# Optimization experiments

Hardware: AMD Instinct MI355X
Metric: run time of the kernel (lower is better)

## Reference

```python
import jax, jax.numpy as jnp
import numpy as np

SHARP = 50.0  # softness of the analytic brush edge


def _rasterize(param, dec, ps):
    # param: [N,12], dec: [N] float 0/1 -> fg,[N,3,ps,ps] (color*alpha*dec), alpha [N,3,ps,ps]
    p = jax.nn.sigmoid(param[:, :8])
    x0, y0 = p[:, 0], p[:, 1]
    wd = jnp.maximum(p[:, 2], 1e-2)
    ht = jnp.maximum(p[:, 3], 1e-2)
    theta = p[:, 4] * jnp.pi
    color = p[:, 5:8]
    lin = (jnp.arange(ps, dtype=param.dtype) + 0.5) / ps
    gy, gx = jnp.meshgrid(lin, lin, indexing='ij')            # [ps,ps]
    dx = gx[None] - x0[:, None, None]
    dy = gy[None] - y0[:, None, None]
    ct = jnp.cos(theta)[:, None, None]
    st = jnp.sin(theta)[:, None, None]
    u = dx * ct + dy * st
    v = -dx * st + dy * ct
    alpha = (jax.nn.sigmoid(SHARP * (wd[:, None, None] / 2 - jnp.abs(u)))
             * jax.nn.sigmoid(SHARP * (ht[:, None, None] / 2 - jnp.abs(v))))
    alpha = alpha * dec[:, None, None]                         # masked scatter == multiply
    alpha3 = jnp.broadcast_to(alpha[:, None], (alpha.shape[0], 3, ps, ps))
    fg = color[:, :, None, None] * alpha3                      # foreground*alpha pre-fused
    return fg, alpha3


def reference(param, decision, cur_canvas):
    b, h, w, s, _ = param.shape
    H, W = cur_canvas.shape[-2], cur_canvas.shape[-1]
    ps = 2 * H // h  # patch_size (== 2*W//w)
    dec = decision.astype(cur_canvas.dtype).reshape(-1)
    fg, al = _rasterize(param.reshape(-1, 12), dec, ps)
    fg = fg.reshape(b, h, w, s, 3, ps, ps)
    al = al.reshape(b, h, w, s, 3, ps, ps)
    q = ps // 4
    canvas = jnp.pad(cur_canvas, ((0, 0), (0, 0), (q, q), (q, q)))
    ey, ex = np.arange(0, h, 2), np.arange(0, w, 2)
    oy, ox = np.arange(1, h, 2), np.arange(1, w, 2)

    def blend(cv, rows, cols, off_y, off_x):
        ny, nx = len(rows), len(cols)
        region = cv[:, :, off_y:off_y + ny * ps, off_x:off_x + nx * ps]
        tiles = region.reshape(b, 3, ny, ps, nx, ps).transpose(0, 2, 4, 1, 3, 5)  # [b,ny,nx,3,ps,ps]
        sf = fg[:, rows][:, :, cols]   # [b,ny,nx,s,3,ps,ps]
        sa = al[:, rows][:, :, cols]
        for i in range(s):
            tiles = sf[:, :, :, i] + tiles * (1.0 - sa[:, :, :, i])
        region = tiles.transpose(0, 3, 1, 4, 2, 5).reshape(b, 3, ny * ps, nx * ps)
        return cv.at[:, :, off_y:off_y + ny * ps, off_x:off_x + nx * ps].set(region)

    canvas = blend(canvas, ey, ex, 0, 0)
    canvas = blend(canvas, oy, ox, ps // 2, ps // 2)
    canvas = blend(canvas, oy, ex, ps // 2, 0)
    canvas = blend(canvas, ey, ox, 0, ps // 2)
    return canvas[:, :, q:-q, q:-q]


def setup_inputs() -> dict:
    key = jax.random.key(0)
    k1, k2, k3 = jax.random.split(key, 3)
    b, h, w, s = 1, 64, 64, 5
    H = W = 1024
    param = jax.random.normal(k1, (b, h, w, s, 12), dtype=jnp.float32)
    decision = jax.random.randint(k2, (b, h, w, s), 0, 2, dtype=jnp.int32)
    cur_canvas = jax.random.uniform(k3, (b, 3, H, W), dtype=jnp.float32)
    return {'param': param, 'decision': decision, 'cur_canvas': cur_canvas}
```

## Files before the change

### kernel.cpp

```cpp
#include <hip/hip_runtime.h>

#define PI_F 3.14159265358979323846f
constexpr float SL = 50.0f * 1.44269504089f;

__device__ __forceinline__ float fexp2(float x) {
#if __has_builtin(__builtin_amdgcn_exp2f)
  return __builtin_amdgcn_exp2f(x);
#else
  return __expf(x * 0.69314718056f);
#endif
}
__device__ __forceinline__ float frcp(float x) {
#if __has_builtin(__builtin_amdgcn_rcpf)
  return __builtin_amdgcn_rcpf(x);
#else
  return 1.0f / x;
#endif
}
__device__ __forceinline__ float fsig(float x) {
  return frcp(1.0f + fexp2(-x * 1.44269504089f));
}

__global__ __launch_bounds__(64) void render_kernel(
    const float* __restrict__ param, const int* __restrict__ dec,
    const float* __restrict__ canvas, float* __restrict__ out) {
  __shared__ float4 lds4[20 * 3];

  const int A = blockIdx.y, B = blockIdx.x;
  const int re = (A & 1) ? A - 1 : A;
  const int ro = (A & 1) ? A : A - 1;
  const int ce = (B & 1) ? B - 1 : B;
  const int co = (B & 1) ? B : B - 1;

  const int j = threadIdx.x;

  bool live = false;
  float4 w0q, w1q, w2q;
  if (j < 20) {
    const int k = j / 5;
    const int i = j - k * 5;
    const int rr = (k == 0 || k == 3) ? re : ro;
    const int cc = (k & 1) ? co : ce;
    if ((unsigned)rr < 64u && (unsigned)cc < 64u) {
      const int tid = rr * 64 + cc;
      const int sid = tid * 5 + i;
      if (dec[sid] != 0) {
        const float4* p4 = (const float4*)(param + (size_t)sid * 12);
        float4 a = p4[0];
        float4 b = p4[1];
        float x0 = fsig(a.x), y0 = fsig(a.y);
        float wd = fmaxf(fsig(a.z), 0.01f);
        float ht = fmaxf(fsig(a.w), 0.01f);
        float th = fsig(b.x) * PI_F;
        float ct = __cosf(th), st = __sinf(th);
        w0q = make_float4((float)(cc * 16) + 32.0f * x0,
                          (float)(rr * 16) + 32.0f * y0,
                          ct * (SL / 32.0f), st * (SL / 32.0f));
        w1q = make_float4(SL * wd * 0.5f, SL * ht * 0.5f,
                          fsig(b.y), fsig(b.z));
        w2q = make_float4(fsig(b.w), 0.0f, 0.0f, 0.0f);
        live = true;
      }
    }
  }
  const unsigned long long mask = __ballot(live);
  const int total = __popcll(mask);
  if (live) {
    const int off = __popcll(mask & ((1ull << j) - 1));
    lds4[off * 3 + 0] = w0q;
    lds4[off * 3 + 1] = w1q;
    lds4[off * 3 + 2] = w2q;
  }
  __syncthreads();

  const int cg = j & 3;
  const int row = j >> 2;
  const int Xb = B * 16 - 8 + cg * 4;
  const int Yr = A * 16 - 8 + row;
  const bool valid = ((unsigned)Xb < 1024u) & ((unsigned)Yr < 1024u);
  if (!valid) return;

  const size_t pix = (size_t)Yr * 1024 + Xb;
  float4 v0 = *(const float4*)(canvas + pix);
  float4 v1 = *(const float4*)(canvas + pix + 1024 * 1024);
  float4 v2 = *(const float4*)(canvas + pix + 2 * 1024 * 1024);

  const float fx0 = (float)(B * 16 + cg * 4) + 0.5f;
  const float fy  = (float)(A * 16 + row) + 0.5f;

  for (int s = 0; s < total; ++s) {
    const float4 qa = lds4[s * 3 + 0];
    const float4 qb = lds4[s * 3 + 1];
    const float4 qc = lds4[s * 3 + 2];
    const float dx0 = fx0 - qa.x;
    const float dy  = fy - qa.y;
    float u = dx0 * qa.z + dy * qa.w;
    float w = dy * qa.z - dx0 * qa.w;
    float* pv0 = &v0.x;
    float* pv1 = &v1.x;
    float* pv2 = &v2.x;
#pragma unroll
    for (int m = 0; m < 4; ++m) {
      const float e1 = fexp2(fabsf(u) - qb.x);
      const float e2 = fexp2(fabsf(w) - qb.y);
      const float al = frcp((1.0f + e1) * (1.0f + e2));
      pv0[m] = fmaf(al, qb.z - pv0[m], pv0[m]);
      pv1[m] = fmaf(al, qb.w - pv1[m], pv1[m]);
      pv2[m] = fmaf(al, qc.x - pv2[m], pv2[m]);
      u += qa.z;
      w -= qa.w;
    }
  }

  *(float4*)(out + pix) = v0;
  *(float4*)(out + pix + 1024 * 1024) = v1;
  *(float4*)(out + pix + 2 * 1024 * 1024) = v2;
}

extern "C" void kernel_launch(void* const* d_in, const int* in_sizes, int n_in,
                              void* d_out, int out_size, void* d_ws, size_t ws_size,
                              hipStream_t stream) {
  const float* param  = (const float*)d_in[0];
  const int*   dec    = (const int*)d_in[1];
  const float* canvas = (const float*)d_in[2];
  float* outp = (float*)d_out;
  (void)d_ws; (void)ws_size;

  dim3 grid(65, 65, 1);
  render_kernel<<<grid, 64, 0, stream>>>(param, dec, canvas, outp);
}
```

Baseline: 79.58 us.

## Cull negligible strokes, remap blocks across XCDs, hoist canvas loads, unroll by two

Each stroke's alpha is now bounded over the 16x16 block, and strokes whose sigmoid product falls below about 2^-20 everywhere are dropped before blending. Block IDs are remapped so each XCD gets a contiguous range of tiles, which should improve L2 locality. Canvas loads are issued before the stroke setup so their latency overlaps it. The stroke loop is unrolled by two so the exp and rcp work of two strokes can interleave. The __syncthreads is replaced by a bare lgkmcnt wait, which is only safe because the block is a single 64-wide wavefront; culling also adds a small approximation error.

```diff
diff --git a/kernel.cpp b/kernel.cpp
--- a/kernel.cpp
+++ b/kernel.cpp
@@ -24,42 +24,74 @@
 __global__ __launch_bounds__(64) void render_kernel(
     const float* __restrict__ param, const int* __restrict__ dec,
     const float* __restrict__ canvas, float* __restrict__ out) {
-  __shared__ float4 lds4[20 * 3];
+  __shared__ float4 ldsA[20];
+  __shared__ float4 ldsB[20];
+  __shared__ float  ldsC[20];
 
-  const int A = blockIdx.y, B = blockIdx.x;
+  const int bid = blockIdx.y * 65 + blockIdx.x;
+  const int xcd = bid & 7;
+  const int idx = bid >> 3;
+  const int rid = (xcd == 0) ? idx : (529 + (xcd - 1) * 528 + idx);
+  const int A = rid / 65;
+  const int B = rid - A * 65;
+
+  const int j = threadIdx.x;
+
+  const int cg = j & 3;
+  const int row = j >> 2;
+  const int Xb = B * 16 - 8 + cg * 4;
+  const int Yr = A * 16 - 8 + row;
+  const bool valid = ((unsigned)Xb < 1024u) & ((unsigned)Yr < 1024u);
+  const size_t pix = (size_t)Yr * 1024 + Xb;
+  float4 v0 = {}, v1 = {}, v2 = {};
+  if (valid) {
+    v0 = *(const float4*)(canvas + pix);
+    v1 = *(const float4*)(canvas + pix + 1024 * 1024);
+    v2 = *(const float4*)(canvas + pix + 2 * 1024 * 1024);
+  }
+
   const int re = (A & 1) ? A - 1 : A;
   const int ro = (A & 1) ? A : A - 1;
   const int ce = (B & 1) ? B - 1 : B;
   const int co = (B & 1) ? B : B - 1;
 
-  const int j = threadIdx.x;
-
   bool live = false;
-  float4 w0q, w1q, w2q;
+  float4 w0q, w1q;
+  float w2s = 0.0f;
   if (j < 20) {
     const int k = j / 5;
     const int i = j - k * 5;
     const int rr = (k == 0 || k == 3) ? re : ro;
     const int cc = (k & 1) ? co : ce;
     if ((unsigned)rr < 64u && (unsigned)cc < 64u) {
-      const int tid = rr * 64 + cc;
-      const int sid = tid * 5 + i;
-      if (dec[sid] != 0) {
-        const float4* p4 = (const float4*)(param + (size_t)sid * 12);
-        float4 a = p4[0];
-        float4 b = p4[1];
-        float x0 = fsig(a.x), y0 = fsig(a.y);
-        float wd = fmaxf(fsig(a.z), 0.01f);
-        float ht = fmaxf(fsig(a.w), 0.01f);
-        float th = fsig(b.x) * PI_F;
-        float ct = __cosf(th), st = __sinf(th);
-        w0q = make_float4((float)(cc * 16) + 32.0f * x0,
-                          (float)(rr * 16) + 32.0f * y0,
-                          ct * (SL / 32.0f), st * (SL / 32.0f));
-        w1q = make_float4(SL * wd * 0.5f, SL * ht * 0.5f,
-                          fsig(b.y), fsig(b.z));
-        w2q = make_float4(fsig(b.w), 0.0f, 0.0f, 0.0f);
-        live = true;
+      const int sid = (rr * 64 + cc) * 5 + i;
+      const int d = dec[sid];
+      const float4* p4 = (const float4*)(param + (size_t)sid * 12);
+      const float4 a = p4[0];
+      const float4 b = p4[1];
+      if (d != 0) {
+        const float x0 = fsig(a.x), y0 = fsig(a.y);
+        const float wd = fmaxf(fsig(a.z), 0.01f);
+        const float ht = fmaxf(fsig(a.w), 0.01f);
+        const float th = fsig(b.x) * PI_F;
+        const float ct = __cosf(th), st = __sinf(th);
+        const float ctp = ct * (SL / 32.0f), stp = st * (SL / 32.0f);
+        const float X0 = (float)(cc * 16) + 32.0f * x0;
+        const float Y0 = (float)(rr * 16) + 32.0f * y0;
+        const float thU = SL * wd * 0.5f, thV = SL * ht * 0.5f;
+        const float dxc = ((float)(B * 16) + 8.0f) - X0;
+        const float dyc = ((float)(A * 16) + 8.0f) - Y0;
+        const float uc = dxc * ctp + dyc * stp;
+        const float vc = dyc * ctp - dxc * stp;
+        const float dd = (fabsf(ctp) + fabsf(stp)) * 7.5f;
+        const float tu = fminf(thU - fabsf(uc) + dd, 0.0f);
+        const float tv = fminf(thV - fabsf(vc) + dd, 0.0f);
+        if (tu + tv >= -20.0f) {
+          w0q = make_float4(X0, Y0, ctp, stp);
+          w1q = make_float4(thU, thV, fsig(b.y), fsig(b.z));
+          w2s = fsig(b.w);
+          live = true;
+        }
       }
     }
   }
@@ -67,38 +99,66 @@
   const int total = __popcll(mask);
   if (live) {
     const int off = __popcll(mask & ((1ull << j) - 1));
-    lds4[off * 3 + 0] = w0q;
-    lds4[off * 3 + 1] = w1q;
-    lds4[off * 3 + 2] = w2q;
+    ldsA[off] = w0q;
+    ldsB[off] = w1q;
+    ldsC[off] = w2s;
   }
-  __syncthreads();
-
-  const int cg = j & 3;
-  const int row = j >> 2;
-  const int Xb = B * 16 - 8 + cg * 4;
-  const int Yr = A * 16 - 8 + row;
-  const bool valid = ((unsigned)Xb < 1024u) & ((unsigned)Yr < 1024u);
+  asm volatile("s_waitcnt lgkmcnt(0)" ::: "memory");
   if (!valid) return;
-
-  const size_t pix = (size_t)Yr * 1024 + Xb;
-  float4 v0 = *(const float4*)(canvas + pix);
-  float4 v1 = *(const float4*)(canvas + pix + 1024 * 1024);
-  float4 v2 = *(const float4*)(canvas + pix + 2 * 1024 * 1024);
 
   const float fx0 = (float)(B * 16 + cg * 4) + 0.5f;
   const float fy  = (float)(A * 16 + row) + 0.5f;
 
-  for (int s = 0; s < total; ++s) {
-    const float4 qa = lds4[s * 3 + 0];
-    const float4 qb = lds4[s * 3 + 1];
-    const float4 qc = lds4[s * 3 + 2];
-    const float dx0 = fx0 - qa.x;
-    const float dy  = fy - qa.y;
+  float* pv0 = &v0.x;
+  float* pv1 = &v1.x;
+  float* pv2 = &v2.x;
+
+  int s = 0;
+  for (; s + 2 <= total; s += 2) {
+    const float4 qa0 = ldsA[s],     qb0 = ldsB[s];
+    const float4 qa1 = ldsA[s + 1], qb1 = ldsB[s + 1];
+    const float  qc0 = ldsC[s],     qc1 = ldsC[s + 1];
+    float al0[4], al1[4];
+    {
+      const float dx0 = fx0 - qa0.x, dy = fy - qa0.y;
+      float u = dx0 * qa0.z + dy * qa0.w;
+      float w = dy * qa0.z - dx0 * qa0.w;
+#pragma unroll
+      for (int m = 0; m < 4; ++m) {
+        const float e1 = fexp2(fabsf(u) - qb0.x);
+        const float e2 = fexp2(fabsf(w) - qb0.y);
+        al0[m] = frcp((1.0f + e1) * (1.0f + e2));
+        u += qa0.z;  w -= qa0.w;
+      }
+    }
+    {
+      const float dx0 = fx0 - qa1.x, dy = fy - qa1.y;
+      float u = dx0 * qa1.z + dy * qa1.w;
+      float w = dy * qa1.z - dx0 * qa1.w;
+#pragma unroll
+      for (int m = 0; m < 4; ++m) {
+        const float e1 = fexp2(fabsf(u) - qb1.x);
+        const float e2 = fexp2(fabsf(w) - qb1.y);
+        al1[m] = frcp((1.0f + e1) * (1.0f + e2));
+        u += qa1.z;  w -= qa1.w;
+      }
+    }
+#pragma unroll
+    for (int m = 0; m < 4; ++m) {
+      pv0[m] = fmaf(al0[m], qb0.z - pv0[m], pv0[m]);
+      pv1[m] = fmaf(al0[m], qb0.w - pv1[m], pv1[m]);
+      pv2[m] = fmaf(al0[m], qc0   - pv2[m], pv2[m]);
+      pv0[m] = fmaf(al1[m], qb1.z - pv0[m], pv0[m]);
+      pv1[m] = fmaf(al1[m], qb1.w - pv1[m], pv1[m]);
+      pv2[m] = fmaf(al1[m], qc1   - pv2[m], pv2[m]);
+    }
+  }
+  if (s < total) {
+    const float4 qa = ldsA[s], qb = ldsB[s];
+    const float  qc = ldsC[s];
+    const float dx0 = fx0 - qa.x, dy = fy - qa.y;
     float u = dx0 * qa.z + dy * qa.w;
     float w = dy * qa.z - dx0 * qa.w;
-    float* pv0 = &v0.x;
-    float* pv1 = &v1.x;
-    float* pv2 = &v2.x;
 #pragma unroll
     for (int m = 0; m < 4; ++m) {
       const float e1 = fexp2(fabsf(u) - qb.x);
@@ -106,9 +166,8 @@
       const float al = frcp((1.0f + e1) * (1.0f + e2));
       pv0[m] = fmaf(al, qb.z - pv0[m], pv0[m]);
       pv1[m] = fmaf(al, qb.w - pv1[m], pv1[m]);
-      pv2[m] = fmaf(al, qc.x - pv2[m], pv2[m]);
-      u += qa.z;
-      w -= qa.w;
+      pv2[m] = fmaf(al, qc   - pv2[m], pv2[m]);
+      u += qa.z;  w -= qa.w;
     }
   }
 
```

Result: no change. 78.15 us (-1.8%).
